# Kernel optimization log

Hardware: AMD Instinct MI355X
Metric: run time of the kernel (lower is better)

## Reference

```python
import jax, jax.numpy as jnp
import numpy as np

# Module hyperparameters (init_kwargs)
THRESHOLD_ABS = 0.2
THRESHOLD_REL = 0.05   # set to None to disable the relative-threshold branch
MIN_DISTANCE = 3


def setup_inputs() -> dict:
    key = jax.random.key(0)
    # belief maps in [0, 1), NCHW
    belive_map = jax.random.uniform(key, (32, 4, 512, 512), dtype=jnp.float32)
    return {"belive_map": belive_map}


def reference(belive_map):
    """Peak detection on belief maps (dense, jit-friendly form).

    Faithful to BeliveMapsNMS.forward: the torch module additionally compacts
    the mask into (coords, labels, scores) lists via nonzero/gather, which has
    data-dependent shapes; here we return the equivalent dense outputs:
      mask        [B,C,H,W] bool   - peak locations (nonzero of this == torch ind)
      scores_abs  [B,C,H,W] f32    - belief value at peaks, 0 elsewhere
      scores_rel  [B,C,H,W] f32    - scores_abs / per-(b,c) max
    """
    k = 2 * MIN_DISTANCE + 1          # 7
    pad = k // 2                       # 3 -> 'same' max pool, stride 1

    # F.max_pool2d(kernel=k, stride=1, padding=k//2)
    x_max = jax.lax.reduce_window(
        belive_map, -jnp.inf, jax.lax.max,
        window_dimensions=(1, 1, k, k),
        window_strides=(1, 1, 1, 1),
        padding=[(0, 0), (0, 0), (pad, pad), (pad, pad)],
    )

    # per-(batch, channel) global max: hh.max(dim=2) on the flattened map
    vmax = jnp.max(belive_map, axis=(2, 3), keepdims=True)  # [B,C,1,1]

    mask = (x_max == belive_map) & (belive_map > THRESHOLD_ABS)
    if THRESHOLD_REL is not None:
        mask = mask & (belive_map > THRESHOLD_REL * vmax)

    scores_abs = jnp.where(mask, belive_map, jnp.float32(0.0))
    scores_rel = scores_abs / vmax
    return mask, scores_abs, scores_rel
```

## Files before the change

kernel.cpp:

```cpp
#include <hip/hip_runtime.h>
#include <math.h>


#define H 512
#define W 512
#define PLANE_ELEMS (H * W)
#define TH 16
#define LROWS (TH + 6)
#define NEG_INF (-INFINITY)

typedef float v4f __attribute__((ext_vector_type(4)));

__device__ __forceinline__ float4 vmax4(float4 a, float4 b) {
    return make_float4(fmaxf(a.x, b.x), fmaxf(a.y, b.y), fmaxf(a.z, b.z), fmaxf(a.w, b.w));
}

__device__ __forceinline__ void nt_store4(float* p, float a, float b, float c, float d) {
    v4f v = {a, b, c, d};
    __builtin_nontemporal_store(v, (v4f*)p);
}

__global__ __launch_bounds__(256) void vmax_kernel(const float* __restrict__ in,
                                                   unsigned int* __restrict__ vmax_bits) {
    const int q = blockIdx.x;
    const int plane = blockIdx.y;
    const float4* p = (const float4*)(in + (size_t)plane * PLANE_ELEMS + q * (PLANE_ELEMS / 4));
    float m = 0.0f;
    const int nvec = PLANE_ELEMS / 4 / 4;
    for (int i = threadIdx.x; i < nvec; i += 256) {
        float4 v = p[i];
        m = fmaxf(m, fmaxf(fmaxf(v.x, v.y), fmaxf(v.z, v.w)));
    }
    #pragma unroll
    for (int o = 32; o > 0; o >>= 1) m = fmaxf(m, __shfl_down(m, o, 64));
    __shared__ float s[4];
    if ((threadIdx.x & 63) == 0) s[threadIdx.x >> 6] = m;
    __syncthreads();
    if (threadIdx.x == 0) {
        m = fmaxf(fmaxf(s[0], s[1]), fmaxf(s[2], s[3]));
        atomicMax(&vmax_bits[plane], __float_as_uint(m));
    }
}

__global__ __launch_bounds__(256) void nms_kernel(const float* __restrict__ in,
                                                  const unsigned int* __restrict__ vmax_bits,
                                                  float* __restrict__ out, int N) {
    const int hwid = blockIdx.x + (blockIdx.y << 5);
    const int wg = ((hwid & 7) << 9) + (hwid >> 3);
    const int plane = wg >> 5;
    const int ty0 = (wg & 31) * TH;

    const float* pin = in + (size_t)plane * PLANE_ELEMS;

    __shared__ __align__(16) float sRow[LROWS * W];

    const int wid = threadIdx.x >> 6;
    const int lane = threadIdx.x & 63;
    const int c8 = lane << 3;

    float4 va[6], vb[6];
    #pragma unroll
    for (int k = 0; k < 6; ++k) {
        const int r = wid + (k << 2);
        if (r < LROWS) {
            const int gy = ty0 + r - 3;
            if (gy >= 0 && gy < H) {
                const float4* row = (const float4*)(pin + (size_t)gy * W);
                va[k] = row[lane * 2];
                vb[k] = row[lane * 2 + 1];
            } else {
                va[k] = vb[k] = make_float4(NEG_INF, NEG_INF, NEG_INF, NEG_INF);
            }
        }
    }

    #pragma unroll
    for (int k = 0; k < 6; ++k) {
        const int r = wid + (k << 2);
        if (r < LROWS) {
            float4 v0 = va[k], v1 = vb[k];
            float l0 = __shfl_up(v1.y, 1, 64), l1 = __shfl_up(v1.z, 1, 64), l2 = __shfl_up(v1.w, 1, 64);
            float r0 = __shfl_down(v0.x, 1, 64), r1 = __shfl_down(v0.y, 1, 64), r2 = __shfl_down(v0.z, 1, 64);
            if (lane == 0) { l0 = NEG_INF; l1 = NEG_INF; l2 = NEG_INF; }
            if (lane == 63) { r0 = NEG_INF; r1 = NEG_INF; r2 = NEG_INF; }
            float a[14] = {l0, l1, l2, v0.x, v0.y, v0.z, v0.w, v1.x, v1.y, v1.z, v1.w, r0, r1, r2};
            float A[7];
            A[6] = a[6];
            #pragma unroll
            for (int j = 5; j >= 0; --j) A[j] = fmaxf(a[j], A[j + 1]);
            float rm[8];
            rm[0] = A[0];
            float B = a[7];
            rm[1] = fmaxf(A[1], B);
            #pragma unroll
            for (int j = 2; j <= 6; ++j) { B = fmaxf(B, a[6 + j]); rm[j] = fmaxf(A[j], B); }
            B = fmaxf(B, a[13]);
            rm[7] = B;
            float4* dst = (float4*)&sRow[r * W + c8];
            dst[0] = make_float4(rm[0], rm[1], rm[2], rm[3]);
            dst[1] = make_float4(rm[4], rm[5], rm[6], rm[7]);
        }
    }

    const int strip = threadIdx.x >> 7;
    const int cg = threadIdx.x & 127;
    const int c = cg << 2;
    const int y0 = strip << 3;
    const int gy_base = ty0 + y0;

    float4 ctr[8];
    #pragma unroll
    for (int i = 0; i < 8; ++i) {
        ctr[i] = *(const float4*)(pin + (size_t)(gy_base + i) * W + c);
    }

    const float vmax = __uint_as_float(vmax_bits[plane]);
    const float rel_thr = 0.05f * vmax;
    const float inv_vmax = 1.0f / vmax;

    __syncthreads();

    float* __restrict__ omask = out;
    float* __restrict__ oabs = out + (size_t)N;
    float* __restrict__ orel = out + 2 * (size_t)N;

    float4 Lr[7], Aq[7];
    #pragma unroll
    for (int k = 0; k < 7; ++k) Lr[k] = *(const float4*)&sRow[(y0 + k) * W + c];
    Aq[6] = Lr[6];
    #pragma unroll
    for (int j = 5; j >= 0; --j) Aq[j] = vmax4(Lr[j], Aq[j + 1]);

    float4 Bq;
    #pragma unroll
    for (int i = 0; i < 8; ++i) {
        float4 m;
        if (i == 0) {
            m = Aq[0];
        } else {
            float4 row = *(const float4*)&sRow[(y0 + 6 + i) * W + c];
            Bq = (i == 1) ? row : vmax4(Bq, row);
            m = (i == 7) ? Bq : vmax4(Aq[i], Bq);
        }
        const int gy = gy_base + i;
        const float4 cc = ctr[i];
        const bool p0 = (m.x == cc.x) & (cc.x > 0.2f) & (cc.x > rel_thr);
        const bool p1 = (m.y == cc.y) & (cc.y > 0.2f) & (cc.y > rel_thr);
        const bool p2 = (m.z == cc.z) & (cc.z > 0.2f) & (cc.z > rel_thr);
        const bool p3 = (m.w == cc.w) & (cc.w > 0.2f) & (cc.w > rel_thr);
        const float a0 = p0 ? cc.x : 0.0f, a1 = p1 ? cc.y : 0.0f;
        const float a2 = p2 ? cc.z : 0.0f, a3 = p3 ? cc.w : 0.0f;
        const size_t o = (size_t)plane * PLANE_ELEMS + (size_t)gy * W + c;
        nt_store4(omask + o, p0 ? 1.0f : 0.0f, p1 ? 1.0f : 0.0f,
                             p2 ? 1.0f : 0.0f, p3 ? 1.0f : 0.0f);
        nt_store4(oabs + o, a0, a1, a2, a3);
        nt_store4(orel + o, a0 * inv_vmax, a1 * inv_vmax, a2 * inv_vmax, a3 * inv_vmax);
    }
}

extern "C" void kernel_launch(void* const* d_in, const int* in_sizes, int n_in,
                              void* d_out, int out_size, void* d_ws, size_t ws_size,
                              hipStream_t stream) {
    const float* in = (const float*)d_in[0];
    float* out = (float*)d_out;
    const int N = in_sizes[0];
    const int planes = N / PLANE_ELEMS;

    unsigned int* vmax_bits = (unsigned int*)d_ws;
    (void)hipMemsetAsync(vmax_bits, 0, planes * sizeof(unsigned int), stream);

    vmax_kernel<<<dim3(4, planes), 256, 0, stream>>>(in, vmax_bits);
    nms_kernel<<<dim3(H / TH, planes), 256, 0, stream>>>(in, vmax_bits, out, N);
}
```

Baseline: 486.6 us.

## Replace atomic vmax with per-chunk partials and halve NMS tile height

The plane-max kernel now splits each plane into 16 chunks, and each block loads 16 float4 per thread up front, then writes a partial max to workspace. This removes the memset and the atomicMax. The NMS kernel reduces the 16 partials itself and uses 8-row tiles instead of 16, which doubles the block count and uses less LDS per block, with launch bounds requesting 4 blocks per SIMD. The trade-off is more halo re-reads: 14 rows loaded per 8 output rows instead of 22 per 16.

```diff
diff --git a/kernel.cpp b/kernel.cpp
--- a/kernel.cpp
+++ b/kernel.cpp
@@ -5,9 +5,10 @@
 #define H 512
 #define W 512
 #define PLANE_ELEMS (H * W)
-#define TH 16
+#define TH 8
 #define LROWS (TH + 6)
 #define NEG_INF (-INFINITY)
+#define VCHUNKS 16
 
 typedef float v4f __attribute__((ext_vector_type(4)));
 
@@ -21,34 +22,37 @@
 }
 
 __global__ __launch_bounds__(256) void vmax_kernel(const float* __restrict__ in,
-                                                   unsigned int* __restrict__ vmax_bits) {
-    const int q = blockIdx.x;
+                                                   float* __restrict__ partials) {
+    const int chunk = blockIdx.x;
     const int plane = blockIdx.y;
-    const float4* p = (const float4*)(in + (size_t)plane * PLANE_ELEMS + q * (PLANE_ELEMS / 4));
-    float m = 0.0f;
-    const int nvec = PLANE_ELEMS / 4 / 4;
-    for (int i = threadIdx.x; i < nvec; i += 256) {
-        float4 v = p[i];
-        m = fmaxf(m, fmaxf(fmaxf(v.x, v.y), fmaxf(v.z, v.w)));
-    }
+    const float4* p = (const float4*)(in + (size_t)plane * PLANE_ELEMS) + chunk * 4096;
+    float4 v[16];
+    #pragma unroll
+    for (int j = 0; j < 16; ++j) v[j] = p[threadIdx.x + (j << 8)];
+    float4 t[8];
+    #pragma unroll
+    for (int j = 0; j < 8; ++j) t[j] = vmax4(v[j], v[j + 8]);
+    #pragma unroll
+    for (int j = 0; j < 4; ++j) t[j] = vmax4(t[j], t[j + 4]);
+    float4 q = vmax4(vmax4(t[0], t[1]), vmax4(t[2], t[3]));
+    float m = fmaxf(fmaxf(q.x, q.y), fmaxf(q.z, q.w));
     #pragma unroll
     for (int o = 32; o > 0; o >>= 1) m = fmaxf(m, __shfl_down(m, o, 64));
     __shared__ float s[4];
     if ((threadIdx.x & 63) == 0) s[threadIdx.x >> 6] = m;
     __syncthreads();
     if (threadIdx.x == 0) {
-        m = fmaxf(fmaxf(s[0], s[1]), fmaxf(s[2], s[3]));
-        atomicMax(&vmax_bits[plane], __float_as_uint(m));
+        partials[(plane << 4) + chunk] = fmaxf(fmaxf(s[0], s[1]), fmaxf(s[2], s[3]));
     }
 }
 
-__global__ __launch_bounds__(256) void nms_kernel(const float* __restrict__ in,
-                                                  const unsigned int* __restrict__ vmax_bits,
-                                                  float* __restrict__ out, int N) {
-    const int hwid = blockIdx.x + (blockIdx.y << 5);
-    const int wg = ((hwid & 7) << 9) + (hwid >> 3);
-    const int plane = wg >> 5;
-    const int ty0 = (wg & 31) * TH;
+__global__ __launch_bounds__(256, 4) void nms_kernel(const float* __restrict__ in,
+                                                     const float* __restrict__ partials,
+                                                     float* __restrict__ out, int N) {
+    const int hwid = blockIdx.x + (blockIdx.y << 6);
+    const int wg = ((hwid & 7) << 10) + (hwid >> 3);
+    const int plane = wg >> 6;
+    const int ty0 = (wg & 63) * TH;
 
     const float* pin = in + (size_t)plane * PLANE_ELEMS;
 
@@ -58,9 +62,13 @@
     const int lane = threadIdx.x & 63;
     const int c8 = lane << 3;
 
-    float4 va[6], vb[6];
+    float pm[16];
     #pragma unroll
-    for (int k = 0; k < 6; ++k) {
+    for (int j = 0; j < 16; ++j) pm[j] = partials[(plane << 4) + j];
+
+    float4 va[4], vb[4];
+    #pragma unroll
+    for (int k = 0; k < 4; ++k) {
         const int r = wid + (k << 2);
         if (r < LROWS) {
             const int gy = ty0 + r - 3;
@@ -75,7 +83,7 @@
     }
 
     #pragma unroll
-    for (int k = 0; k < 6; ++k) {
+    for (int k = 0; k < 4; ++k) {
         const int r = wid + (k << 2);
         if (r < LROWS) {
             float4 v0 = va[k], v1 = vb[k];
@@ -105,16 +113,18 @@
     const int strip = threadIdx.x >> 7;
     const int cg = threadIdx.x & 127;
     const int c = cg << 2;
-    const int y0 = strip << 3;
+    const int y0 = strip << 2;
     const int gy_base = ty0 + y0;
 
-    float4 ctr[8];
+    float4 ctr[4];
     #pragma unroll
-    for (int i = 0; i < 8; ++i) {
+    for (int i = 0; i < 4; ++i) {
         ctr[i] = *(const float4*)(pin + (size_t)(gy_base + i) * W + c);
     }
 
-    const float vmax = __uint_as_float(vmax_bits[plane]);
+    float vmax = pm[0];
+    #pragma unroll
+    for (int j = 1; j < 16; ++j) vmax = fmaxf(vmax, pm[j]);
     const float rel_thr = 0.05f * vmax;
     const float inv_vmax = 1.0f / vmax;
 
@@ -124,23 +134,28 @@
     float* __restrict__ oabs = out + (size_t)N;
     float* __restrict__ orel = out + 2 * (size_t)N;
 
-    float4 Lr[7], Aq[7];
+    float4 Lr[7];
     #pragma unroll
     for (int k = 0; k < 7; ++k) Lr[k] = *(const float4*)&sRow[(y0 + k) * W + c];
-    Aq[6] = Lr[6];
-    #pragma unroll
-    for (int j = 5; j >= 0; --j) Aq[j] = vmax4(Lr[j], Aq[j + 1]);
+    float4 Aq[4];
+    {
+        float4 suf = vmax4(Lr[4], vmax4(Lr[5], Lr[6]));
+        Aq[3] = vmax4(Lr[3], suf);
+        Aq[2] = vmax4(Lr[2], Aq[3]);
+        Aq[1] = vmax4(Lr[1], Aq[2]);
+        Aq[0] = vmax4(Lr[0], Aq[1]);
+    }
 
     float4 Bq;
     #pragma unroll
-    for (int i = 0; i < 8; ++i) {
+    for (int i = 0; i < 4; ++i) {
         float4 m;
         if (i == 0) {
             m = Aq[0];
         } else {
             float4 row = *(const float4*)&sRow[(y0 + 6 + i) * W + c];
             Bq = (i == 1) ? row : vmax4(Bq, row);
-            m = (i == 7) ? Bq : vmax4(Aq[i], Bq);
+            m = vmax4(Aq[i], Bq);
         }
         const int gy = gy_base + i;
         const float4 cc = ctr[i];
@@ -166,9 +181,8 @@
     const int N = in_sizes[0];
     const int planes = N / PLANE_ELEMS;
 
-    unsigned int* vmax_bits = (unsigned int*)d_ws;
-    (void)hipMemsetAsync(vmax_bits, 0, planes * sizeof(unsigned int), stream);
+    float* partials = (float*)d_ws;
 
-    vmax_kernel<<<dim3(4, planes), 256, 0, stream>>>(in, vmax_bits);
-    nms_kernel<<<dim3(H / TH, planes), 256, 0, stream>>>(in, vmax_bits, out, N);
+    vmax_kernel<<<dim3(VCHUNKS, planes), 256, 0, stream>>>(in, partials);
+    nms_kernel<<<dim3(H / TH, planes), 256, 0, stream>>>(in, partials, out, N);
 }
```

New measurement: 477.1 us. 1.02x faster.
